# Performance work log

Hardware: AMD Instinct MI355X
Metric: run time of the kernel (lower is better)

## Reference

```python
import jax, jax.numpy as jnp
import numpy as np

EPS = 1e-12  # torch F.normalize eps


def setup_inputs() -> dict:
    key = jax.random.key(0)
    k1, k2, k3 = jax.random.split(key, 3)
    b, c, h, w = 4, 192, 128, 128
    num_heads = 8
    in1 = jax.random.normal(k1, (b, c, h, w), dtype=jnp.float32)
    in2 = jax.random.normal(k2, (b, c, h, w), dtype=jnp.float32)
    scale = jnp.ones((num_heads, 1, 1), dtype=jnp.float32)
    proj_w = jax.random.normal(k3, (c, c), dtype=jnp.float32) * (1.0 / np.sqrt(c))
    return {"in1": in1, "in2": in2, "scale": scale, "proj_w": proj_w, "num_heads": num_heads}


def reference(in1, in2, scale, proj_w, num_heads):
    b, c, h, w = in1.shape
    hd = c // num_heads
    hw = h * w
    # b (head c) h w -> b head c (h w)
    q = in1.reshape(b, num_heads, hd, hw)
    k = in2.reshape(b, num_heads, hd, hw)
    # L2-normalize along the (h w) axis, torch eps semantics
    q = q / jnp.maximum(jnp.linalg.norm(q, axis=-1, keepdims=True), EPS)
    k = k / jnp.maximum(jnp.linalg.norm(k, axis=-1, keepdims=True), EPS)
    # channel-wise attention: [b, head, c, c]
    attn = jnp.einsum('bhcn,bhdn->bhcd', q, k) * scale  # scale broadcasts [head,1,1]
    attn = jax.nn.softmax(attn, axis=-1)
    out = jnp.einsum('bhcd,bhdn->bhcn', attn, k)
    out = out.reshape(b, c, h, w)
    # 1x1 conv projection (no bias)
    out = jnp.einsum('oc,bchw->bohw', proj_w, out)
    return out
```

## Files before the change

kernel.cpp:

```cpp
#include <hip/hip_runtime.h>
#include <hip/hip_bf16.h>
#include <math.h>

#define BATCH 4
#define NHEAD 8
#define HD 24
#define CH 192
#define HW 16384
#define SPL 32
#define SROW 640

#define OFF_MO  (32 * SPL * SROW)
#define OFF_CNT (OFF_MO + (BATCH * CH * CH) / 2)

#define LSTR 132

typedef __attribute__((ext_vector_type(8)))  short bf16x8;
typedef __attribute__((ext_vector_type(16))) float f32x16;

__device__ __forceinline__ unsigned short bf16rne(float x) {
    union { float f; unsigned u; } v; v.f = x;
    unsigned u = v.u;
    return (unsigned short)((u + 0x7FFFu + ((u >> 16) & 1u)) >> 16);
}

__device__ __forceinline__ unsigned pack2(float a, float b) {
    union { __hip_bfloat162 h; unsigned u; } c;
    c.h = __float22bfloat162_rn(float2{a, b});
    return c.u;
}

__device__ __forceinline__ void st_agent(float* p, float v) {
    __hip_atomic_store(p, v, __ATOMIC_RELAXED, __HIP_MEMORY_SCOPE_AGENT);
}
__device__ __forceinline__ float ld_agent(const float* p) {
    return __hip_atomic_load(p, __ATOMIC_RELAXED, __HIP_MEMORY_SCOPE_AGENT);
}

__global__ __launch_bounds__(256, 4) void kA(const float* __restrict__ q,
                                             const float* __restrict__ k,
                                             const float* __restrict__ scale,
                                             const float* __restrict__ w,
                                             float* __restrict__ ws,
                                             unsigned short* __restrict__ Mo,
                                             unsigned int* __restrict__ cnt) {
    __shared__ unsigned int tile[2][HD * LSTR];
    __shared__ int lastFlag;

    const int bh   = blockIdx.x;
    const int wn   = (blockIdx.y + bh) & 31;
    const int t    = threadIdx.x;
    const int lane = t & 63;
    const int wave = t >> 6;
    const int m    = lane & 31;
    const int hi   = lane >> 5;
    const int rowc = (m < HD) ? m : 0;

    f32x16 aQK = {}, aQQ = {}, aKK = {};

    #pragma unroll
    for (int half = 0; half < 2; ++half) {
        const float* qb = q + (size_t)bh * HD * HW + wn * 512 + half * 256;
        const float* kb = k + (size_t)bh * HD * HW + wn * 512 + half * 256;

        #pragma unroll
        for (int j = 0; j < 6; ++j) {
            const int idx = j * 256 + t;
            const int row = idx >> 6;
            const int c64 = idx & 63;
            float4 qv = *(const float4*)(qb + (size_t)row * HW + c64 * 4);
            float4 kv = *(const float4*)(kb + (size_t)row * HW + c64 * 4);
            *(uint2*)&tile[0][row * LSTR + c64 * 2] =
                make_uint2(pack2(qv.x, qv.y), pack2(qv.z, qv.w));
            *(uint2*)&tile[1][row * LSTR + c64 * 2] =
                make_uint2(pack2(kv.x, kv.y), pack2(kv.z, kv.w));
        }
        __syncthreads();

        #pragma unroll
        for (int s = 0; s < 4; ++s) {
            const int off = (wave * 64 + s * 16) >> 1;
            bf16x8 aq = *(const bf16x8*)&tile[0][rowc * LSTR + off + hi * 4];
            bf16x8 bk = *(const bf16x8*)&tile[1][rowc * LSTR + off + hi * 4];
            aQK = __builtin_amdgcn_mfma_f32_32x32x16_bf16(aq, bk, aQK, 0, 0, 0);
            aQQ = __builtin_amdgcn_mfma_f32_32x32x16_bf16(aq, aq, aQQ, 0, 0, 0);
            aKK = __builtin_amdgcn_mfma_f32_32x32x16_bf16(bk, bk, aKK, 0, 0, 0);
        }
        __syncthreads();
    }

    float* red = (float*)tile;
    if (m < HD) {
        #pragma unroll
        for (int r = 0; r < 16; ++r) {
            const int i = (r & 3) + 8 * (r >> 2) + 4 * hi;
            if (i < HD) {
                red[wave * 624 + i * HD + m] = aQK[r];
                if (i == m) {
                    red[wave * 624 + 576 + i] = aQQ[r];
                    red[wave * 624 + 600 + i] = aKK[r];
                }
            }
        }
    }
    __syncthreads();

    float* Srow = ws + ((size_t)bh * SPL + wn) * SROW;
    for (int e = t; e < 624; e += 256)
        st_agent(&Srow[e], red[e] + red[624 + e] + red[1248 + e] + red[1872 + e]);

    asm volatile("s_waitcnt vmcnt(0)" ::: "memory");
    __syncthreads();

    if (t == 0) {
        unsigned int old = __hip_atomic_fetch_add(&cnt[bh], 1u,
                                                  __ATOMIC_RELAXED,
                                                  __HIP_MEMORY_SCOPE_AGENT);
        lastFlag = (old == SPL - 1);
    }
    __syncthreads();
    if (!lastFlag) return;

    float* sf = (float*)tile;
    const int b = bh >> 3;
    const int h = bh & 7;
    const float* base = ws + (size_t)bh * SPL * SROW;

    for (int idx = t; idx < CH * HD; idx += 256) {
        int o = idx / HD, dd = idx - o * HD;
        sf[672 + idx] = w[o * CH + h * HD + dd];
    }
    for (int e = t; e < 624; e += 256) {
        float s0 = 0.f, s1 = 0.f, s2 = 0.f, s3 = 0.f;
        #pragma unroll
        for (int sp = 0; sp < SPL; sp += 4) {
            s0 += ld_agent(&base[(size_t)(sp + 0) * SROW + e]);
            s1 += ld_agent(&base[(size_t)(sp + 1) * SROW + e]);
            s2 += ld_agent(&base[(size_t)(sp + 2) * SROW + e]);
            s3 += ld_agent(&base[(size_t)(sp + 3) * SROW + e]);
        }
        sf[e] = (s0 + s1) + (s2 + s3);
    }
    __syncthreads();

    if (t < 2 * HD) {
        float inv = 1.0f / fmaxf(sqrtf(sf[576 + t]), 1e-12f);
        sf[624 + t] = inv;
    }
    __syncthreads();

    const float sc = scale[h];
    for (int e = t; e < 576; e += 256)
        sf[e] = sf[e] * sf[624 + e / HD] * sf[648 + e % HD] * sc;
    __syncthreads();

    if (t < HD) {
        float mx = -1e30f;
        for (int j = 0; j < HD; ++j) mx = fmaxf(mx, sf[t * HD + j]);
        float sum = 0.f;
        for (int j = 0; j < HD; ++j) {
            float v = expf(sf[t * HD + j] - mx);
            sf[t * HD + j] = v;
            sum += v;
        }
        float r = 1.0f / sum;
        for (int j = 0; j < HD; ++j) sf[t * HD + j] *= r;
    }
    __syncthreads();

    for (int idx = t; idx < CH * HD; idx += 256) {
        int o = idx / HD, j = idx - o * HD;
        float v = 0.f;
        #pragma unroll
        for (int i = 0; i < HD; ++i)
            v = fmaf(sf[672 + o * HD + i], sf[i * HD + j], v);
        Mo[(size_t)b * CH * CH + (size_t)o * CH + h * HD + j] = bf16rne(v * sf[648 + j]);
    }
}

#define KCN 64
#define BSTR3 100

__global__ __launch_bounds__(256, 4) void kC(const float* __restrict__ k,
                                             const unsigned short* __restrict__ Mo,
                                             float* __restrict__ out) {
    __shared__ unsigned int Bt[KCN * BSTR3];

    const int t    = threadIdx.x;
    const int lane = t & 63;
    const int wave = t >> 6;
    const int n31  = lane & 31;
    const int hi   = lane >> 5;
    const int nt   = wave & 1;
    const int otb  = (wave >> 1) * 3;

    const int nb = blockIdx.x * KCN;
    const int b  = blockIdx.y;

    const float* kb = k + (size_t)b * CH * HW;
    const unsigned short* Mob = Mo + (size_t)b * CH * CH;

    const int np4 = t & 15;
    const int cg4 = t >> 4;

    #pragma unroll
    for (int s = 0; s < 3; ++s) {
        float4 v[4];
        #pragma unroll
        for (int cc = 0; cc < 4; ++cc)
            v[cc] = *(const float4*)(kb + (size_t)(s * 64 + cg4 * 4 + cc) * HW + nb + np4 * 4);
        #pragma unroll
        for (int r = 0; r < 4; ++r) {
            float x0 = (&v[0].x)[r], x1 = (&v[1].x)[r];
            float x2 = (&v[2].x)[r], x3 = (&v[3].x)[r];
            *(uint2*)&Bt[(np4 * 4 + r) * BSTR3 + s * 32 + cg4 * 2] =
                make_uint2(pack2(x0, x1), pack2(x2, x3));
        }
    }
    __syncthreads();

    f32x16 acc[3] = {};
    #pragma unroll
    for (int kc = 0; kc < 12; ++kc) {
        bf16x8 Bf = *(const bf16x8*)&Bt[(nt * 32 + n31) * BSTR3 + kc * 8 + hi * 4];
        #pragma unroll
        for (int oi = 0; oi < 3; ++oi) {
            const unsigned short* ap =
                Mob + (size_t)((otb + oi) * 32 + n31) * CH + kc * 16 + hi * 8;
            bf16x8 Af = *(const bf16x8*)ap;
            acc[oi] = __builtin_amdgcn_mfma_f32_32x32x16_bf16(Af, Bf, acc[oi], 0, 0, 0);
        }
    }

    float* op = out + (size_t)b * CH * HW;
    const int n = nb + nt * 32 + n31;
    #pragma unroll
    for (int oi = 0; oi < 3; ++oi)
        #pragma unroll
        for (int r = 0; r < 16; ++r) {
            int o = (otb + oi) * 32 + (r & 3) + 8 * (r >> 2) + 4 * hi;
            op[(size_t)o * HW + n] = acc[oi][r];
        }
}

extern "C" void kernel_launch(void* const* d_in, const int* in_sizes, int n_in,
                              void* d_out, int out_size, void* d_ws, size_t ws_size,
                              hipStream_t stream) {
    const float* in1   = (const float*)d_in[0];
    const float* in2   = (const float*)d_in[1];
    const float* scale = (const float*)d_in[2];
    const float* projw = (const float*)d_in[3];
    float* ws  = (float*)d_ws;
    float* out = (float*)d_out;
    unsigned short* Mo = (unsigned short*)(ws + OFF_MO);
    unsigned int* cnt  = (unsigned int*)(ws + OFF_CNT);

    hipMemsetAsync((void*)cnt, 0, 32 * sizeof(unsigned int), stream);
    kA<<<dim3(32, SPL), 256, 0, stream>>>(in1, in2, scale, projw, ws, Mo, cnt);
    kC<<<dim3(HW / KCN, BATCH), 256, 0, stream>>>(in2, Mo, out);
}
```

Measured before the change: 174.4 us.

## Cache bf16-converted K in workspace so projection kernel reads half the bytes

The first kernel now writes the bf16-packed K tile it already builds into a workspace buffer. The second kernel reads that bf16 copy instead of re-reading fp32 K from global memory and converting it again, which halves its input traffic. The cost is an extra 25 MB write in the first kernel and scalar 2-byte LDS transpose stores in the second. The block index remap that staggered column blocks per head is also removed.

```diff
diff --git a/kernel.cpp b/kernel.cpp
--- a/kernel.cpp
+++ b/kernel.cpp
@@ -12,6 +12,7 @@
 
 #define OFF_MO  (32 * SPL * SROW)
 #define OFF_CNT (OFF_MO + (BATCH * CH * CH) / 2)
+#define OFF_KBF 729600
 
 #define LSTR 132
 
@@ -43,12 +44,13 @@
                                              const float* __restrict__ w,
                                              float* __restrict__ ws,
                                              unsigned short* __restrict__ Mo,
-                                             unsigned int* __restrict__ cnt) {
+                                             unsigned int* __restrict__ cnt,
+                                             unsigned int* __restrict__ kbf) {
     __shared__ unsigned int tile[2][HD * LSTR];
     __shared__ int lastFlag;
 
     const int bh   = blockIdx.x;
-    const int wn   = (blockIdx.y + bh) & 31;
+    const int cb   = blockIdx.y;
     const int t    = threadIdx.x;
     const int lane = t & 63;
     const int wave = t >> 6;
@@ -60,8 +62,8 @@
 
     #pragma unroll
     for (int half = 0; half < 2; ++half) {
-        const float* qb = q + (size_t)bh * HD * HW + wn * 512 + half * 256;
-        const float* kb = k + (size_t)bh * HD * HW + wn * 512 + half * 256;
+        const float* qb = q + (size_t)bh * HD * HW + cb * 512 + half * 256;
+        const float* kb = k + (size_t)bh * HD * HW + cb * 512 + half * 256;
 
         #pragma unroll
         for (int j = 0; j < 6; ++j) {
@@ -70,10 +72,12 @@
             const int c64 = idx & 63;
             float4 qv = *(const float4*)(qb + (size_t)row * HW + c64 * 4);
             float4 kv = *(const float4*)(kb + (size_t)row * HW + c64 * 4);
-            *(uint2*)&tile[0][row * LSTR + c64 * 2] =
-                make_uint2(pack2(qv.x, qv.y), pack2(qv.z, qv.w));
-            *(uint2*)&tile[1][row * LSTR + c64 * 2] =
-                make_uint2(pack2(kv.x, kv.y), pack2(kv.z, kv.w));
+            uint2 qp = make_uint2(pack2(qv.x, qv.y), pack2(qv.z, qv.w));
+            uint2 kp = make_uint2(pack2(kv.x, kv.y), pack2(kv.z, kv.w));
+            *(uint2*)&tile[0][row * LSTR + c64 * 2] = qp;
+            *(uint2*)&tile[1][row * LSTR + c64 * 2] = kp;
+            kbf[(((size_t)(bh * HD + row)) << 13) + (cb << 8) + half * 128 + (c64 << 1)]     = kp.x;
+            kbf[(((size_t)(bh * HD + row)) << 13) + (cb << 8) + half * 128 + (c64 << 1) + 1] = kp.y;
         }
         __syncthreads();
 
@@ -105,7 +109,7 @@
     }
     __syncthreads();
 
-    float* Srow = ws + ((size_t)bh * SPL + wn) * SROW;
+    float* Srow = ws + ((size_t)bh * SPL + cb) * SROW;
     for (int e = t; e < 624; e += 256)
         st_agent(&Srow[e], red[e] + red[624 + e] + red[1248 + e] + red[1872 + e]);
 
@@ -181,7 +185,7 @@
 #define KCN 64
 #define BSTR3 100
 
-__global__ __launch_bounds__(256, 4) void kC(const float* __restrict__ k,
+__global__ __launch_bounds__(256, 4) void kC(const unsigned int* __restrict__ kbf,
                                              const unsigned short* __restrict__ Mo,
                                              float* __restrict__ out) {
     __shared__ unsigned int Bt[KCN * BSTR3];
@@ -197,25 +201,19 @@
     const int nb = blockIdx.x * KCN;
     const int b  = blockIdx.y;
 
-    const float* kb = k + (size_t)b * CH * HW;
     const unsigned short* Mob = Mo + (size_t)b * CH * CH;
 
-    const int np4 = t & 15;
-    const int cg4 = t >> 4;
-
-    #pragma unroll
-    for (int s = 0; s < 3; ++s) {
-        float4 v[4];
-        #pragma unroll
-        for (int cc = 0; cc < 4; ++cc)
-            v[cc] = *(const float4*)(kb + (size_t)(s * 64 + cg4 * 4 + cc) * HW + nb + np4 * 4);
-        #pragma unroll
-        for (int r = 0; r < 4; ++r) {
-            float x0 = (&v[0].x)[r], x1 = (&v[1].x)[r];
-            float x2 = (&v[2].x)[r], x3 = (&v[3].x)[r];
-            *(uint2*)&Bt[(np4 * 4 + r) * BSTR3 + s * 32 + cg4 * 2] =
-                make_uint2(pack2(x0, x1), pack2(x2, x3));
-        }
+    unsigned short* bt16 = (unsigned short*)Bt;
+    #pragma unroll
+    for (int i = 0; i < 6; ++i) {
+        const int idx = i * 256 + t;
+        const int ch  = idx >> 3;
+        const int sl  = idx & 7;
+        uint4 v4 = *(const uint4*)(kbf + (((size_t)(b * CH + ch)) << 13) +
+                                   ((size_t)blockIdx.x << 5) + (sl << 2));
+        #pragma unroll
+        for (int jj = 0; jj < 8; ++jj)
+            bt16[(sl * 8 + jj) * (BSTR3 * 2) + ch] = ((const unsigned short*)&v4)[jj];
     }
     __syncthreads();
 
@@ -254,8 +252,9 @@
     float* out = (float*)d_out;
     unsigned short* Mo = (unsigned short*)(ws + OFF_MO);
     unsigned int* cnt  = (unsigned int*)(ws + OFF_CNT);
+    unsigned int* kbf  = (unsigned int*)(ws + OFF_KBF);
 
     hipMemsetAsync((void*)cnt, 0, 32 * sizeof(unsigned int), stream);
-    kA<<<dim3(32, SPL), 256, 0, stream>>>(in1, in2, scale, projw, ws, Mo, cnt);
-    kC<<<dim3(HW / KCN, BATCH), 256, 0, stream>>>(in2, Mo, out);
-}
+    kA<<<dim3(32, SPL), 256, 0, stream>>>(in1, in2, scale, projw, ws, Mo, cnt, kbf);
+    kC<<<dim3(HW / KCN, BATCH), 256, 0, stream>>>(kbf, Mo, out);
+}
```

Result: no change. 176.1 us (+1.0%).
